# Kernel tuning notes

Hardware: AMD Instinct MI355X
Metric: run time of the kernel (lower is better)

Reference implementation:

```python
import jax, jax.numpy as jnp
import numpy as np

B, H, L, D = 8, 12, 2048, 64
E = H * D            # 768 = state_size = hidden_size
K, S, P = 3, 2, 1    # conv kernel, stride, padding (2P - K = -1 matches avg_pool residual)


def setup_inputs() -> dict:
    key = jax.random.key(0)
    ks = jax.random.split(key, 8)
    init = lambda k, shape: jax.random.normal(k, shape, jnp.float32) * 0.02
    return {
        "state": jax.random.normal(ks[0], (B, H, L, D), jnp.float32),
        # input_proj Linear(E,E)
        "Wi": init(ks[1], (E, E)), "bi": jnp.zeros((E,), jnp.float32),
        # ConvMultiheadAttention: strided Conv1d query proj, stored as [K, E_in, E_out]
        "Wq": init(ks[2], (K, E, E)), "bq": jnp.zeros((E,), jnp.float32),
        "Wk": init(ks[3], (E, E)), "bk": jnp.zeros((E,), jnp.float32),
        "Wv": init(ks[4], (E, E)), "bv": jnp.zeros((E,), jnp.float32),
        "Wao": init(ks[5], (E, E)), "bao": jnp.zeros((E,), jnp.float32),  # attn out_proj
        # output_proj Linear(E,E)
        "Wo": init(ks[6], (E, E)), "bo": jnp.zeros((E,), jnp.float32),
    }


def reference(state, Wi, bi, Wq, bq, Wk, bk, Wv, bv, Wao, bao, Wo, bo):
    b, h, l, d = state.shape
    e = h * d
    # [B,H,L,D] -> [B,L,H*D]
    x = state.transpose(0, 2, 1, 3).reshape(b, l, e)
    residual = x
    # input projection + ReLU
    x = jax.nn.relu(x @ Wi.T + bi)
    # strided convolutional query projection: [B,L,E] -> [B,Lq,E]
    q = jax.lax.conv_general_dilated(
        x, Wq, window_strides=(S,), padding=[(P, P)],
        dimension_numbers=("NWC", "WIO", "NWC")) + bq
    k = x @ Wk.T + bk
    v = x @ Wv.T + bv
    lq = q.shape[1]
    qh = q.reshape(b, lq, h, d)
    kh = k.reshape(b, l, h, d)
    vh = v.reshape(b, l, h, d)
    scale = 1.0 / jnp.sqrt(jnp.asarray(d, x.dtype))
    scores = jnp.einsum("bqhd,bkhd->bhqk", qh, kh) * scale  # [B,H,Lq,L]
    attn = jax.nn.softmax(scores, axis=-1)
    o = jnp.einsum("bhqk,bkhd->bqhd", attn, vh).reshape(b, lq, e)
    o = o @ Wao.T + bao          # attention out_proj
    o = jax.nn.relu(o)
    o = o @ Wo.T + bo            # output projection
    # avg_pool1d with kernel=1, stride=S, pad=0 == strided subsampling
    o = o + residual[:, ::S, :]
    # [B,Lq,E] -> [B,H,Lq,D]
    out = o.reshape(b, lq, h, d).transpose(0, 2, 1, 3)
    return out
```

## Files before the change

### kernel.cpp

```cpp
#include <hip/hip_runtime.h>
#include <hip/hip_bf16.h>
#include <stdint.h>

#define DEVI __device__ __forceinline__

typedef short s8v __attribute__((ext_vector_type(8)));
typedef short s4v __attribute__((ext_vector_type(4)));
typedef float f4v __attribute__((ext_vector_type(4)));

DEVI short f2bf(float f) {
  unsigned u = __builtin_bit_cast(unsigned, f);
  u += 0x7FFFu + ((u >> 16) & 1u);
  return (short)(u >> 16);
}

DEVI unsigned cvtpk(float lo, float hi) {
  unsigned r;
  asm("v_cvt_pk_bf16_f32 %0, %1, %2" : "=v"(r) : "v"(lo), "v"(hi));
  return r;
}

DEVI void gload16(const void* g, void* l) {
  __builtin_amdgcn_global_load_lds((const __attribute__((address_space(1))) unsigned*)g,
                                   (__attribute__((address_space(3))) unsigned*)l,
                                   16, 0, 0);
}


__global__ __launch_bounds__(256) void k_tr_state(const float* __restrict__ st,
                                                  short* __restrict__ xbf) {
  int idx = blockIdx.x * 256 + threadIdx.x;
  int dc = idx & 7;
  int l  = (idx >> 3) & 2047;
  int hb = idx >> 14;
  int h = hb % 12, b = hb / 12;
  const float* s = st + ((size_t)hb * 2048 + l) * 64 + dc * 8;
  f4v a = *(const f4v*)s;
  f4v c = *(const f4v*)(s + 4);
  short o[8];
#pragma unroll
  for (int j = 0; j < 4; ++j) { o[j] = f2bf(a[j]); o[4 + j] = f2bf(c[j]); }
  *(s8v*)(xbf + ((size_t)(b * 2048 + l)) * 768 + h * 64 + dc * 8) = *(s8v*)o;
}

__global__ __launch_bounds__(256) void k_castw(const float* __restrict__ src,
                                               short* __restrict__ dst, float sc) {
  int idx = blockIdx.x * 256 + threadIdx.x;
  const float* s = src + (size_t)idx * 8;
  f4v a = *(const f4v*)s;
  f4v c = *(const f4v*)(s + 4);
  short o[8];
#pragma unroll
  for (int j = 0; j < 4; ++j) { o[j] = f2bf(a[j] * sc); o[4 + j] = f2bf(c[j] * sc); }
  *(s8v*)(dst + (size_t)idx * 8) = *(s8v*)o;
}

__global__ __launch_bounds__(256) void k_bkv(const float* __restrict__ bk,
                                             const float* __restrict__ bv,
                                             float* __restrict__ bkv) {
  int i = blockIdx.x * 256 + threadIdx.x;
  bkv[i] = (i < 768) ? bk[i] * 0.125f : bv[i - 768];
}

__global__ __launch_bounds__(256) void k_tr_wq(const float* __restrict__ wq,
                                               short* __restrict__ wqt) {
  __shared__ float tile[32][33];
  const int kw = blockIdx.z;
  const int i0 = blockIdx.y * 32, o0 = blockIdx.x * 32;
  const int tx = threadIdx.x & 31, ty = threadIdx.x >> 5;
#pragma unroll
  for (int rr = 0; rr < 32; rr += 8)
    tile[ty + rr][tx] = wq[((size_t)kw * 768 + i0 + ty + rr) * 768 + o0 + tx];
  __syncthreads();
#pragma unroll
  for (int rr = 0; rr < 32; rr += 8)
    wqt[(size_t)(o0 + ty + rr) * 2304 + kw * 768 + i0 + tx] = f2bf(tile[tx][ty + rr]);
}

__global__ __launch_bounds__(256) void k_tr_v(const short* __restrict__ v,
                                              short* __restrict__ vt, int vs) {
  __shared__ short tile[32][33];
  const int bh = blockIdx.z;
  const int l0 = blockIdx.x * 32, d0 = blockIdx.y * 32;
  const int b = bh / 12, h = bh % 12;
  const int tx = threadIdx.x & 31, ty = threadIdx.x >> 5;
#pragma unroll
  for (int rr = 0; rr < 32; rr += 8)
    tile[ty + rr][tx] = v[((size_t)(b * 2048 + l0 + ty + rr)) * vs + h * 64 + d0 + tx];
  __syncthreads();
#pragma unroll
  for (int rr = 0; rr < 32; rr += 8)
    vt[((size_t)(bh * 64 + d0 + ty + rr)) * 2048 + l0 + tx] = tile[tx][ty + rr];
}

template <int AMODE, int EPI>
__global__ __launch_bounds__(256, 2)
void k_gemm(const short* __restrict__ A, const short* __restrict__ Bt,
            const float* __restrict__ bias, short* __restrict__ Cbf,
            float* __restrict__ Cf, const float* __restrict__ st,
            const short* __restrict__ zp, int M, int N, int K) {
  __shared__ __align__(16) short As[128 * 32];
  __shared__ __align__(16) short Bs[128 * 32];
  const int tid = threadIdx.x;
  const int w = tid >> 6, l = tid & 63;
  const int g = l >> 4, r = l & 15;

  const int nwg = gridDim.x * gridDim.y;
  const int lin = blockIdx.y * gridDim.x + blockIdx.x;
  const int lin2 = (lin & 7) * (nwg >> 3) + (lin >> 3);
  const int m0 = (lin2 / gridDim.x) * 128, n0 = (lin2 % gridDim.x) * 128;
  const int wm = w >> 1, wn = w & 1;

  f4v acc[4][4] = {};

  const int srow = 16 * w + (l >> 2);
  const int sc8 = 8 * (l & 3);

  const int nsteps = K >> 5;
  for (int ks = 0; ks < nsteps; ++ks) {
    const int kk = ks << 5;
    __syncthreads();
    if (AMODE == 0) {
      const short* a0 = A + ((size_t)(m0 + srow) * K + kk + sc8);
      gload16(a0, (char*)As + w * 1024);
      gload16(a0 + (size_t)64 * K, (char*)As + w * 1024 + 4096);
    } else {
      const int kw = ks / 24;
      const int ii = (ks - kw * 24) * 32 + sc8;
#pragma unroll
      for (int j = 0; j < 2; ++j) {
        int m = m0 + srow + 64 * j;
        int b = m >> 10, t = m & 1023;
        int lpos = 2 * t - 1 + kw;
        const short* a0 = (lpos < 0) ? (zp + sc8)
                                     : A + ((size_t)(b * 2048 + lpos) * 768 + ii);
        gload16(a0, (char*)As + w * 1024 + j * 4096);
      }
    }
    {
      const short* b0 = Bt + ((size_t)(n0 + srow) * K + kk + sc8);
      gload16(b0, (char*)Bs + w * 1024);
      gload16(b0 + (size_t)64 * K, (char*)Bs + w * 1024 + 4096);
    }
    __syncthreads();
    s8v af[4], bfr[4];
#pragma unroll
    for (int mt = 0; mt < 4; ++mt)
      af[mt] = *(const s8v*)&As[(64 * wm + 16 * mt + r) * 32 + 8 * g];
#pragma unroll
    for (int nt = 0; nt < 4; ++nt)
      bfr[nt] = *(const s8v*)&Bs[(64 * wn + 16 * nt + r) * 32 + 8 * g];
#pragma unroll
    for (int mt = 0; mt < 4; ++mt)
#pragma unroll
      for (int nt = 0; nt < 4; ++nt)
        acc[mt][nt] = __builtin_amdgcn_mfma_f32_16x16x32_bf16(af[mt], bfr[nt],
                                                              acc[mt][nt], 0, 0, 0);
  }
#pragma unroll
  for (int nt = 0; nt < 4; ++nt) {
    const int col = n0 + 64 * wn + 16 * nt + r;
    const float bv = bias[col];
#pragma unroll
    for (int mt = 0; mt < 4; ++mt) {
#pragma unroll
      for (int i = 0; i < 4; ++i) {
        int row = m0 + 64 * wm + 16 * mt + 4 * g + i;
        float v = acc[mt][nt][i] + bv;
        if (EPI == 0) v = fmaxf(v, 0.f);
        if (EPI <= 1) {
          Cbf[(size_t)row * N + col] = f2bf(v);
        } else {
          int b = row >> 10, t = row & 1023;
          int h = col >> 6, dd = col & 63;
          float res = st[(((size_t)(b * 12 + h) * 2048) + 2 * t) * 64 + dd];
          Cf[(((size_t)(b * 12 + h) * 1024) + t) * 64 + dd] = v + res;
        }
      }
    }
  }
}

__global__ __launch_bounds__(256, 4)
void k_attn(const short* __restrict__ qb, const short* __restrict__ kvb,
            const short* __restrict__ vt, short* __restrict__ ob) {
  __shared__ __align__(16) short Ks[2][64 * 64];
  __shared__ __align__(16) short Vts[2][64 * 64];
  __shared__ __align__(16) short Ps[4][16 * 64];

  const int lin = blockIdx.x;
  const int blk = (lin & 7) * 192 + (lin >> 3);
  const int qblk = blk & 15, bh = blk >> 4;
  const int b = bh / 12, h = bh % 12;
  const int tid = threadIdx.x;
  const int w = tid >> 6, l = tid & 63;
  const int g = l >> 4, r = l & 15;
  const int row = tid >> 3, p = tid & 7;

  const short* qrow = qb + ((size_t)(b * 1024 + qblk * 64 + 16 * w + r)) * 768 + h * 64;
  s8v qf[2];
  qf[0] = *(const s8v*)(qrow + 8 * g);
  qf[1] = *(const s8v*)(qrow + 32 + 8 * g);

  unsigned* pswr[8];
#pragma unroll
  for (int k = 0; k < 8; ++k) {
    const int nt = k >> 1, t = k & 1;
    pswr[k] = (unsigned*)&Ps[w][r * 64 + 8 * ((2 * nt + (g >> 1) + r) & 7) +
                               4 * (g & 1) + 2 * t];
  }
  const s8v* psrd[2];
#pragma unroll
  for (int kc = 0; kc < 2; ++kc)
    psrd[kc] = (const s8v*)&Ps[w][r * 64 + 8 * ((4 * kc + g + r) & 7)];

  auto STAGE = [&](int buf, int jb) {
#pragma unroll
    for (int iss = 0; iss < 2; ++iss) {
      int jr = row + 32 * iss;
      int c = p ^ (jr & 7);
      gload16(kvb + ((size_t)(b * 2048 + jb * 64 + jr)) * 1536 + h * 64 + 8 * c,
              (char*)Ks[buf] + iss * 4096 + w * 1024);
      gload16(vt + ((size_t)(bh * 64 + jr)) * 2048 + jb * 64 + 8 * c,
              (char*)Vts[buf] + iss * 4096 + w * 1024);
    }
  };

  f4v oacc[4] = {};
  float mrun = -3.0e38f, lrun = 0.f;

  STAGE(0, 0);
  asm volatile("s_waitcnt vmcnt(0)" ::: "memory");
  __builtin_amdgcn_s_barrier();

  for (int jb = 0; jb < 32; ++jb) {
    const int cur = jb & 1;
    if (jb < 31) STAGE(cur ^ 1, jb + 1);

    f4v sacc[4] = {};
#pragma unroll
    for (int nt = 0; nt < 4; ++nt)
#pragma unroll
      for (int c = 0; c < 2; ++c) {
        s8v kf = *(const s8v*)&Ks[cur][(16 * nt + r) * 64 + 8 * ((4 * c + g) ^ (r & 7))];
        sacc[nt] = __builtin_amdgcn_mfma_f32_16x16x32_bf16(kf, qf[c], sacc[nt], 0, 0, 0);
      }

    float s[16];
#pragma unroll
    for (int nt = 0; nt < 4; ++nt)
#pragma unroll
      for (int i = 0; i < 4; ++i) s[4 * nt + i] = sacc[nt][i];
    float m01 = fmaxf(fmaxf(s[0], s[1]), fmaxf(s[2], s[3]));
    float m23 = fmaxf(fmaxf(s[4], s[5]), fmaxf(s[6], s[7]));
    float m45 = fmaxf(fmaxf(s[8], s[9]), fmaxf(s[10], s[11]));
    float m67 = fmaxf(fmaxf(s[12], s[13]), fmaxf(s[14], s[15]));
    float mx = fmaxf(fmaxf(m01, m23), fmaxf(m45, m67));
    mx = fmaxf(mx, __shfl_xor(mx, 16));
    mx = fmaxf(mx, __shfl_xor(mx, 32));

    bool defer = __all(mx <= mrun + 8.0f);
    float mn = defer ? mrun : fmaxf(mrun, mx);
    float alpha = defer ? 1.0f : __expf(mrun - mn);
    mrun = mn;

    float ls = 0.f;
#pragma unroll
    for (int k = 0; k < 8; ++k) {
      float p0 = __expf(s[2 * k] - mn);
      float p1 = __expf(s[2 * k + 1] - mn);
      ls += p0 + p1;
      *pswr[k] = cvtpk(p0, p1);
    }
    ls += __shfl_xor(ls, 16);
    ls += __shfl_xor(ls, 32);
    lrun = lrun * alpha + ls;
    if (!defer) {
#pragma unroll
      for (int mt = 0; mt < 4; ++mt)
#pragma unroll
        for (int i = 0; i < 4; ++i) oacc[mt][i] *= alpha;
    }

    asm volatile("" ::: "memory");
    s8v pf0 = *psrd[0], pf1 = *psrd[1];
#pragma unroll
    for (int mt = 0; mt < 4; ++mt) {
      s8v vf0 = *(const s8v*)&Vts[cur][(16 * mt + r) * 64 + 8 * ((g) ^ (r & 7))];
      s8v vf1 = *(const s8v*)&Vts[cur][(16 * mt + r) * 64 + 8 * ((4 + g) ^ (r & 7))];
      oacc[mt] = __builtin_amdgcn_mfma_f32_16x16x32_bf16(vf0, pf0, oacc[mt], 0, 0, 0);
      oacc[mt] = __builtin_amdgcn_mfma_f32_16x16x32_bf16(vf1, pf1, oacc[mt], 0, 0, 0);
    }

    asm volatile("s_waitcnt vmcnt(0)" ::: "memory");
    __builtin_amdgcn_s_barrier();
  }

  const float inv = 1.f / lrun;
  short* obase = ob + ((size_t)(b * 1024 + qblk * 64 + 16 * w + r)) * 768 + h * 64;
#pragma unroll
  for (int mt = 0; mt < 4; ++mt) {
    uint2 uu;
    uu.x = cvtpk(oacc[mt][0] * inv, oacc[mt][1] * inv);
    uu.y = cvtpk(oacc[mt][2] * inv, oacc[mt][3] * inv);
    *(uint2*)(obase + 16 * mt + 4 * g) = uu;
  }
}

extern "C" void kernel_launch(void* const* d_in, const int* in_sizes, int n_in,
                              void* d_out, int out_size, void* d_ws, size_t ws_size,
                              hipStream_t stream) {
  const float* state = (const float*)d_in[0];
  const float* Wi  = (const float*)d_in[1];
  const float* bi  = (const float*)d_in[2];
  const float* Wq  = (const float*)d_in[3];
  const float* bq  = (const float*)d_in[4];
  const float* Wk  = (const float*)d_in[5];
  const float* bk  = (const float*)d_in[6];
  const float* Wv  = (const float*)d_in[7];
  const float* bv  = (const float*)d_in[8];
  const float* Wao = (const float*)d_in[9];
  const float* bao = (const float*)d_in[10];
  const float* Wo  = (const float*)d_in[11];
  const float* bo  = (const float*)d_in[12];
  float* out = (float*)d_out;

  char* ws = (char*)d_ws;
  const size_t SZ = (size_t)16384 * 768 * 2;
  short* xbf = (short*)ws;
  short* y   = (short*)(ws + SZ);
  short* kvbf = (short*)(ws + 2 * SZ);
  short* qbf = (short*)(ws + 4 * SZ);
  char*  wp  = ws + 4 * SZ + SZ / 2;
  short* wib  = (short*)wp;
  short* wkb  = (short*)(wp + 1 * 1179648);
  short* wvb  = (short*)(wp + 2 * 1179648);
  short* waob = (short*)(wp + 3 * 1179648);
  short* wob  = (short*)(wp + 4 * 1179648);
  short* wqt  = (short*)(wp + 5 * 1179648);
  short* zp   = (short*)(wp + 5 * 1179648 + 3538944);
  float* bkv  = (float*)(wp + 5 * 1179648 + 3538944 + 512);
  short* vtb   = xbf;
  short* attno = y;
  short* z1    = (short*)((char*)y + SZ / 2);

  hipMemsetAsync(zp, 0, 256, stream);
  k_tr_state<<<6144, 256, 0, stream>>>(state, xbf);
  k_castw<<<288, 256, 0, stream>>>(Wi, wib, 1.0f);
  k_castw<<<288, 256, 0, stream>>>(Wk, wkb, 0.125f);
  k_castw<<<288, 256, 0, stream>>>(Wv, wvb, 1.0f);
  k_castw<<<288, 256, 0, stream>>>(Wao, waob, 1.0f);
  k_castw<<<288, 256, 0, stream>>>(Wo, wob, 1.0f);
  k_bkv<<<6, 256, 0, stream>>>(bk, bv, bkv);
  k_tr_wq<<<dim3(24, 24, 3), 256, 0, stream>>>(Wq, wqt);

  k_gemm<0, 0><<<dim3(6, 128), 256, 0, stream>>>(xbf, wib, bi, y, nullptr, nullptr, zp, 16384, 768, 768);
  k_gemm<0, 1><<<dim3(12, 128), 256, 0, stream>>>(y, wkb, bkv, kvbf, nullptr, nullptr, zp, 16384, 1536, 768);
  k_gemm<1, 1><<<dim3(6, 64), 256, 0, stream>>>(y, wqt, bq, qbf, nullptr, nullptr, zp, 8192, 768, 2304);
  k_tr_v<<<dim3(64, 2, 96), 256, 0, stream>>>(kvbf + 768, vtb, 1536);
  k_attn<<<1536, 256, 0, stream>>>(qbf, kvbf, vtb, attno);
  k_gemm<0, 0><<<dim3(6, 64), 256, 0, stream>>>(attno, waob, bao, z1, nullptr, nullptr, zp, 8192, 768, 768);
  k_gemm<0, 2><<<dim3(6, 64), 256, 0, stream>>>(z1, wob, bo, nullptr, out, state, zp, 8192, 768, 768);
}
```

Measured before the change: 423.9 us.

## Fuse weight-prep launches and streamline attention softmax with exp2 and single V buffer

Merges five weight casts, the bias prep and the zero-pad memset into one launch to cut launch overhead. In attention, log2(e) is folded into the K scale so the softmax can use raw v_exp_f32, and the deferred-max threshold is widened to match. The per-tile row-sum shuffles are moved to the end, and V is single-buffered, loaded at the start of each tile, to lower LDS use and allow 5 blocks per CU. It also adds s_setprio around the MFMA sections. The risk is that V load latency is now exposed within each iteration.

```diff
diff --git a/kernel.cpp b/kernel.cpp
--- a/kernel.cpp
+++ b/kernel.cpp
@@ -7,6 +7,9 @@
 typedef short s8v __attribute__((ext_vector_type(8)));
 typedef short s4v __attribute__((ext_vector_type(4)));
 typedef float f4v __attribute__((ext_vector_type(4)));
+
+#define KSCALE 0.18033688011112042f
+#define DEFTHR 11.5415603f
 
 DEVI short f2bf(float f) {
   unsigned u = __builtin_bit_cast(unsigned, f);
@@ -17,6 +20,12 @@
 DEVI unsigned cvtpk(float lo, float hi) {
   unsigned r;
   asm("v_cvt_pk_bf16_f32 %0, %1, %2" : "=v"(r) : "v"(lo), "v"(hi));
+  return r;
+}
+
+DEVI float exp2a(float x) {
+  float r;
+  asm volatile("v_exp_f32 %0, %1\n\ts_nop 1" : "=v"(r) : "v"(x));
   return r;
 }
 
@@ -43,23 +52,41 @@
   *(s8v*)(xbf + ((size_t)(b * 2048 + l)) * 768 + h * 64 + dc * 8) = *(s8v*)o;
 }
 
-__global__ __launch_bounds__(256) void k_castw(const float* __restrict__ src,
-                                               short* __restrict__ dst, float sc) {
-  int idx = blockIdx.x * 256 + threadIdx.x;
-  const float* s = src + (size_t)idx * 8;
-  f4v a = *(const f4v*)s;
-  f4v c = *(const f4v*)(s + 4);
-  short o[8];
-#pragma unroll
-  for (int j = 0; j < 4; ++j) { o[j] = f2bf(a[j] * sc); o[4 + j] = f2bf(c[j] * sc); }
-  *(s8v*)(dst + (size_t)idx * 8) = *(s8v*)o;
-}
-
-__global__ __launch_bounds__(256) void k_bkv(const float* __restrict__ bk,
-                                             const float* __restrict__ bv,
-                                             float* __restrict__ bkv) {
-  int i = blockIdx.x * 256 + threadIdx.x;
-  bkv[i] = (i < 768) ? bk[i] * 0.125f : bv[i - 768];
+__global__ __launch_bounds__(256) void k_prep_w(
+    const float* __restrict__ Wi, const float* __restrict__ Wk,
+    const float* __restrict__ Wv, const float* __restrict__ Wao,
+    const float* __restrict__ Wo, const float* __restrict__ bk,
+    const float* __restrict__ bv, short* __restrict__ wib,
+    short* __restrict__ wkb, short* __restrict__ wvb,
+    short* __restrict__ waob, short* __restrict__ wob,
+    float* __restrict__ bkv, short* __restrict__ zp) {
+  const int bid = blockIdx.x;
+  if (bid < 1440) {
+    const int sel = bid / 288, off = bid % 288;
+    const float* src;
+    short* dst;
+    float sc = 1.0f;
+    switch (sel) {
+      case 0: src = Wi;  dst = wib;  break;
+      case 1: src = Wk;  dst = wkb;  sc = KSCALE; break;
+      case 2: src = Wv;  dst = wvb;  break;
+      case 3: src = Wao; dst = waob; break;
+      default: src = Wo; dst = wob;  break;
+    }
+    const int idx = off * 256 + threadIdx.x;
+    const float* s = src + (size_t)idx * 8;
+    f4v a = *(const f4v*)s;
+    f4v c = *(const f4v*)(s + 4);
+    short o[8];
+#pragma unroll
+    for (int j = 0; j < 4; ++j) { o[j] = f2bf(a[j] * sc); o[4 + j] = f2bf(c[j] * sc); }
+    *(s8v*)(dst + (size_t)idx * 8) = *(s8v*)o;
+  } else if (bid < 1446) {
+    const int i = (bid - 1440) * 256 + threadIdx.x;
+    bkv[i] = (i < 768) ? bk[i] * KSCALE : bv[i - 768];
+  } else {
+    zp[threadIdx.x] = 0;
+  }
 }
 
 __global__ __launch_bounds__(256) void k_tr_wq(const float* __restrict__ wq,
@@ -181,11 +208,11 @@
   }
 }
 
-__global__ __launch_bounds__(256, 4)
+__global__ __launch_bounds__(256, 5)
 void k_attn(const short* __restrict__ qb, const short* __restrict__ kvb,
             const short* __restrict__ vt, short* __restrict__ ob) {
   __shared__ __align__(16) short Ks[2][64 * 64];
-  __shared__ __align__(16) short Vts[2][64 * 64];
+  __shared__ __align__(16) short Vts[64 * 64];
   __shared__ __align__(16) short Ps[4][16 * 64];
 
   const int lin = blockIdx.x;
@@ -214,30 +241,39 @@
   for (int kc = 0; kc < 2; ++kc)
     psrd[kc] = (const s8v*)&Ps[w][r * 64 + 8 * ((4 * kc + g + r) & 7)];
 
-  auto STAGE = [&](int buf, int jb) {
+  auto STAGEK = [&](int buf, int jb) {
 #pragma unroll
     for (int iss = 0; iss < 2; ++iss) {
       int jr = row + 32 * iss;
       int c = p ^ (jr & 7);
       gload16(kvb + ((size_t)(b * 2048 + jb * 64 + jr)) * 1536 + h * 64 + 8 * c,
               (char*)Ks[buf] + iss * 4096 + w * 1024);
+    }
+  };
+  auto STAGEV = [&](int jb) {
+#pragma unroll
+    for (int iss = 0; iss < 2; ++iss) {
+      int jr = row + 32 * iss;
+      int c = p ^ (jr & 7);
       gload16(vt + ((size_t)(bh * 64 + jr)) * 2048 + jb * 64 + 8 * c,
-              (char*)Vts[buf] + iss * 4096 + w * 1024);
+              (char*)Vts + iss * 4096 + w * 1024);
     }
   };
 
   f4v oacc[4] = {};
   float mrun = -3.0e38f, lrun = 0.f;
 
-  STAGE(0, 0);
+  STAGEK(0, 0);
   asm volatile("s_waitcnt vmcnt(0)" ::: "memory");
   __builtin_amdgcn_s_barrier();
 
   for (int jb = 0; jb < 32; ++jb) {
     const int cur = jb & 1;
-    if (jb < 31) STAGE(cur ^ 1, jb + 1);
+    STAGEV(jb);
+    if (jb < 31) STAGEK(cur ^ 1, jb + 1);
 
     f4v sacc[4] = {};
+    __builtin_amdgcn_s_setprio(1);
 #pragma unroll
     for (int nt = 0; nt < 4; ++nt)
 #pragma unroll
@@ -245,57 +281,63 @@
         s8v kf = *(const s8v*)&Ks[cur][(16 * nt + r) * 64 + 8 * ((4 * c + g) ^ (r & 7))];
         sacc[nt] = __builtin_amdgcn_mfma_f32_16x16x32_bf16(kf, qf[c], sacc[nt], 0, 0, 0);
       }
+    __builtin_amdgcn_s_setprio(0);
 
     float s[16];
 #pragma unroll
     for (int nt = 0; nt < 4; ++nt)
 #pragma unroll
       for (int i = 0; i < 4; ++i) s[4 * nt + i] = sacc[nt][i];
-    float m01 = fmaxf(fmaxf(s[0], s[1]), fmaxf(s[2], s[3]));
-    float m23 = fmaxf(fmaxf(s[4], s[5]), fmaxf(s[6], s[7]));
-    float m45 = fmaxf(fmaxf(s[8], s[9]), fmaxf(s[10], s[11]));
-    float m67 = fmaxf(fmaxf(s[12], s[13]), fmaxf(s[14], s[15]));
-    float mx = fmaxf(fmaxf(m01, m23), fmaxf(m45, m67));
-    mx = fmaxf(mx, __shfl_xor(mx, 16));
-    mx = fmaxf(mx, __shfl_xor(mx, 32));
-
-    bool defer = __all(mx <= mrun + 8.0f);
-    float mn = defer ? mrun : fmaxf(mrun, mx);
-    float alpha = defer ? 1.0f : __expf(mrun - mn);
-    mrun = mn;
+    float m0 = fmaxf(fmaxf(s[0], s[1]), s[2]);
+    float m1 = fmaxf(fmaxf(s[3], s[4]), s[5]);
+    float m2 = fmaxf(fmaxf(s[6], s[7]), s[8]);
+    float m3 = fmaxf(fmaxf(s[9], s[10]), s[11]);
+    float m4 = fmaxf(fmaxf(s[12], s[13]), s[14]);
+    float mloc = fmaxf(fmaxf(fmaxf(m0, m1), fmaxf(m2, m3)), fmaxf(m4, s[15]));
+
+    float mn = mrun;
+    if (!__all(mloc <= mrun + DEFTHR)) {
+      float mx = mloc;
+      mx = fmaxf(mx, __shfl_xor(mx, 16));
+      mx = fmaxf(mx, __shfl_xor(mx, 32));
+      mn = fmaxf(mrun, mx);
+      float alpha = exp2a(mrun - mn);
+      mrun = mn;
+#pragma unroll
+      for (int mt = 0; mt < 4; ++mt)
+#pragma unroll
+        for (int i = 0; i < 4; ++i) oacc[mt][i] *= alpha;
+      lrun *= alpha;
+    }
 
     float ls = 0.f;
 #pragma unroll
     for (int k = 0; k < 8; ++k) {
-      float p0 = __expf(s[2 * k] - mn);
-      float p1 = __expf(s[2 * k + 1] - mn);
+      float p0 = exp2a(s[2 * k] - mn);
+      float p1 = exp2a(s[2 * k + 1] - mn);
       ls += p0 + p1;
       *pswr[k] = cvtpk(p0, p1);
     }
-    ls += __shfl_xor(ls, 16);
-    ls += __shfl_xor(ls, 32);
-    lrun = lrun * alpha + ls;
-    if (!defer) {
-#pragma unroll
-      for (int mt = 0; mt < 4; ++mt)
-#pragma unroll
-        for (int i = 0; i < 4; ++i) oacc[mt][i] *= alpha;
-    }
-
+    lrun += ls;
+
+    asm volatile("s_waitcnt vmcnt(0)" ::: "memory");
     asm volatile("" ::: "memory");
     s8v pf0 = *psrd[0], pf1 = *psrd[1];
+    __builtin_amdgcn_s_setprio(1);
 #pragma unroll
     for (int mt = 0; mt < 4; ++mt) {
-      s8v vf0 = *(const s8v*)&Vts[cur][(16 * mt + r) * 64 + 8 * ((g) ^ (r & 7))];
-      s8v vf1 = *(const s8v*)&Vts[cur][(16 * mt + r) * 64 + 8 * ((4 + g) ^ (r & 7))];
+      s8v vf0 = *(const s8v*)&Vts[(16 * mt + r) * 64 + 8 * ((g) ^ (r & 7))];
+      s8v vf1 = *(const s8v*)&Vts[(16 * mt + r) * 64 + 8 * ((4 + g) ^ (r & 7))];
       oacc[mt] = __builtin_amdgcn_mfma_f32_16x16x32_bf16(vf0, pf0, oacc[mt], 0, 0, 0);
       oacc[mt] = __builtin_amdgcn_mfma_f32_16x16x32_bf16(vf1, pf1, oacc[mt], 0, 0, 0);
     }
-
-    asm volatile("s_waitcnt vmcnt(0)" ::: "memory");
+    __builtin_amdgcn_s_setprio(0);
+
     __builtin_amdgcn_s_barrier();
   }
 
+  lrun += __shfl_xor(lrun, 16);
+  lrun += __shfl_xor(lrun, 32);
   const float inv = 1.f / lrun;
   short* obase = ob + ((size_t)(b * 1024 + qblk * 64 + 16 * w + r)) * 768 + h * 64;
 #pragma unroll
@@ -344,14 +386,9 @@
   short* attno = y;
   short* z1    = (short*)((char*)y + SZ / 2);
 
-  hipMemsetAsync(zp, 0, 256, stream);
   k_tr_state<<<6144, 256, 0, stream>>>(state, xbf);
-  k_castw<<<288, 256, 0, stream>>>(Wi, wib, 1.0f);
-  k_castw<<<288, 256, 0, stream>>>(Wk, wkb, 0.125f);
-  k_castw<<<288, 256, 0, stream>>>(Wv, wvb, 1.0f);
-  k_castw<<<288, 256, 0, stream>>>(Wao, waob, 1.0f);
-  k_castw<<<288, 256, 0, stream>>>(Wo, wob, 1.0f);
-  k_bkv<<<6, 256, 0, stream>>>(bk, bv, bkv);
+  k_prep_w<<<1447, 256, 0, stream>>>(Wi, Wk, Wv, Wao, Wo, bk, bv,
+                                     wib, wkb, wvb, waob, wob, bkv, zp);
   k_tr_wq<<<dim3(24, 24, 3), 256, 0, stream>>>(Wq, wqt);
 
   k_gemm<0, 0><<<dim3(6, 128), 256, 0, stream>>>(xbf, wib, bi, y, nullptr, nullptr, zp, 16384, 768, 768);
```

New measurement: 409.4 us. 1.04x faster.
